# Optimization experiments

Hardware: AMD Instinct MI355X
Metric: run time of the kernel (lower is better)

Reference implementation:

```python
import jax, jax.numpy as jnp
import numpy as np

N, C, CI, H, W = 64, 512, 256, 12, 4
EPS = 1e-5


def _conv1x1(v, w, b=None):
    # v: [n, cin, h, w], w: [cout, cin]
    o = jnp.einsum('nchw,oc->nohw', v, w)
    if b is not None:
        o = o + b[None, :, None, None]
    return o


def _layernorm(v, g, b):
    # normalize over (C, H, W) per sample, affine params shaped [C, H, W]
    mu = v.mean(axis=(1, 2, 3), keepdims=True)
    var = v.var(axis=(1, 2, 3), keepdims=True)
    return (v - mu) / jnp.sqrt(var + EPS) * g[None] + b[None]


def setup_inputs() -> dict:
    key = jax.random.key(0)
    ks = jax.random.split(key, 12)
    s = 0.02
    return {
        'x': jax.random.normal(ks[0], (N, C, H, W), dtype=jnp.float32),
        'theta_w': jax.random.normal(ks[1], (CI, C), dtype=jnp.float32) * s,
        'theta_b': jnp.zeros((CI,), dtype=jnp.float32),
        'phi_w': jax.random.normal(ks[2], (CI, C), dtype=jnp.float32) * s,
        'phi_b': jnp.zeros((CI,), dtype=jnp.float32),
        'conv1_w': jax.random.normal(ks[3], (C, C), dtype=jnp.float32) * s,
        'conv2_w': jax.random.normal(ks[4], (C, C), dtype=jnp.float32) * s,
        'ln1_g': jnp.ones((C, H, W), dtype=jnp.float32),
        'ln1_b': jnp.zeros((C, H, W), dtype=jnp.float32),
        'ln2_g': jnp.ones((C, H, W), dtype=jnp.float32),
        'ln2_b': jnp.zeros((C, H, W), dtype=jnp.float32),
    }


def reference(x, theta_w, theta_b, phi_w, phi_b, conv1_w, conv2_w,
              ln1_g, ln1_b, ln2_g, ln2_b):
    n = x.shape[0]
    hw = H * W
    # 1x1 conv projections (conv is per-sample, so compute once on the N nodes
    # instead of on the N^2 gathered copies -- identical math)
    theta = _conv1x1(x, theta_w, theta_b)          # [N, CI, H, W]  (gallery proj)
    phi = _conv1x1(x, phi_w, phi_b)                # [N, CI, H, W]  (query proj)
    # MaxPool2d(2,2) on phi -> [N, CI, 6, 2] -> [N, CI, 12]
    phi_p = phi.reshape(n, CI, H // 2, 2, W // 2, 2).max(axis=(3, 5))
    phi_p = phi_p.reshape(n, CI, -1)               # [N, CI, 12]
    t = theta.reshape(n, CI, hw).transpose(0, 2, 1)  # [N, HW, CI]
    # f[i, j] = theta(x[j]) @ pooled phi(x[i]), norm='size' divides by 12
    f = jnp.einsum('jsc,icm->ijsm', t, phi_p) / phi_p.shape[-1]  # [Nq, Ng, HW, 12]
    m = f.max(axis=-1)                             # [Nq, Ng, HW]; max instead of softmax-sum
    # all-pairs layout p = i*N + j: qs[p] = i, gs[p] = j (torch.where row-major)
    gs = jnp.tile(jnp.arange(n), n)                # [N*N]
    # masked gallery image z = x[gs] * attention map, then scatter_add over gs
    z = x[gs] * m.reshape(n * n, 1, H, W)          # [N*N, C, H, W]
    x2 = jax.ops.segment_sum(z, gs, num_segments=n)
    # postprocessing (dropouts are identity at p=0)
    x = x2 + x                                     # res1
    x = _layernorm(x, ln1_g, ln1_b)
    h = _conv1x1(jax.nn.relu(_conv1x1(x, conv1_w)), conv2_w)
    x = x + h                                      # res2
    x = _layernorm(x, ln2_g, ln2_b)
    return x
```

## Files before the change

### kernel.cpp

```cpp
#include <hip/hip_runtime.h>
#include <hip/hip_bf16.h>

#define NN 64
#define CC 512
#define HW 48
#define LNSZ (CC * HW)

typedef __attribute__((ext_vector_type(8))) short bf16x8;
typedef __attribute__((ext_vector_type(4))) float floatx4;

static const size_t WB_OFF   = 0;
static const size_t BC_OFF   = 393216;
static const size_t S_OFF    = 393728;
static const size_t SMU_OFF  = 396800;
static const size_t SRS_OFF  = 396864;
static const size_t CXP_OFF  = 396928;
static const size_t CX2_OFF  = 409216;
static const size_t ST2_OFF  = 421504;
static const size_t XB_OFF   = 422016;
static const size_t TP_OFF   = 1208448;
static const size_t YB_OFF   = 1994880;
static const size_t UB_OFF   = 2781312;
static const size_t PP_OFF   = 3567744;
static const size_t YY_OFF   = 3666048;
static const size_t VV_OFF   = 5238912;

__device__ __forceinline__ void block_reduce2(float& sum, float& sq) {
  const int lane = threadIdx.x & 63, w = threadIdx.x >> 6;
#pragma unroll
  for (int off = 32; off > 0; off >>= 1) {
    sum += __shfl_down(sum, off, 64);
    sq  += __shfl_down(sq, off, 64);
  }
  __shared__ float rs[4], rq[4];
  if (lane == 0) { rs[w] = sum; rq[w] = sq; }
  __syncthreads();
  if (threadIdx.x == 0) {
    sum = rs[0] + rs[1] + rs[2] + rs[3];
    sq  = rq[0] + rq[1] + rq[2] + rq[3];
  }
}

__global__ __launch_bounds__(256) void prep_w(
    const float* __restrict__ tw, const float* __restrict__ pw,
    const float* __restrict__ c1, const float* __restrict__ c2,
    const float* __restrict__ tb, const float* __restrict__ pb,
    __hip_bfloat16* __restrict__ Wb, float* __restrict__ bcat,
    float* __restrict__ S) {
  int g = blockIdx.x * 256 + threadIdx.x;
  float v;
  if (g < 131072)      v = tw[g];
  else if (g < 262144) v = pw[g - 131072];
  else if (g < 524288) v = c1[g - 262144];
  else                 v = c2[g - 524288];
  Wb[g] = __float2bfloat16(v);
  if (g < 512) bcat[g] = g < 256 ? tb[g] : pb[g - 256];
  if (g < 3072) S[g] = 0.f;
}

__global__ __launch_bounds__(256) void trx_stats(
    const float* __restrict__ x, __hip_bfloat16* __restrict__ xb,
    float* __restrict__ cxp, float* __restrict__ cx2p) {
  const int bx = blockIdx.x;
  const int n  = blockIdx.y;
  const int t  = threadIdx.x;
  __shared__ float ts[128 * 49];
  __shared__ float ps[192], pq[192];
  const float* src = x + (size_t)n * LNSZ + (size_t)bx * 128 * HW;
#pragma unroll
  for (int k = 0; k < 6; ++k) {
    int idx = t + k * 256;
    float4 v = ((const float4*)src)[idx];
    int c = idx / 12, sq = (idx % 12) * 4;
    float* d = ts + c * 49 + sq;
    d[0] = v.x; d[1] = v.y; d[2] = v.z; d[3] = v.w;
  }
  __syncthreads();
  if (t < 192) {
    int s = t % 48, q = t / 48;
    float sum = 0.f, sq2 = 0.f;
#pragma unroll
    for (int c = q * 32; c < q * 32 + 32; ++c) {
      float v = ts[c * 49 + s];
      sum += v; sq2 += v * v;
    }
    ps[t] = sum; pq[t] = sq2;
  }
  __hip_bfloat16* dst = xb + (size_t)n * LNSZ + bx * 128;
#pragma unroll
  for (int k = 0; k < 12; ++k) {
    int idx = t + k * 256;
    int s = idx >> 6, cp = idx & 63;
    __hip_bfloat162 p;
    p.x = __float2bfloat16(ts[(cp * 2) * 49 + s]);
    p.y = __float2bfloat16(ts[(cp * 2 + 1) * 49 + s]);
    *(__hip_bfloat162*)(dst + (size_t)s * 512 + cp * 2) = p;
  }
  __syncthreads();
  if (t < 48) {
    cxp[((size_t)n * 4 + bx) * 48 + t] = ps[t] + ps[48 + t] + ps[96 + t] + ps[144 + t];
    cx2p[((size_t)n * 4 + bx) * 48 + t] = pq[t] + pq[48 + t] + pq[96 + t] + pq[144 + t];
  }
}

__global__ __launch_bounds__(256) void gemm_bf16out(
    const __hip_bfloat16* __restrict__ Wb, const __hip_bfloat16* __restrict__ inb,
    const float* __restrict__ bias, __hip_bfloat16* __restrict__ outb, int relu) {
  const int oc = blockIdx.x, n = blockIdx.y;
  const int w = threadIdx.x >> 6, lane = threadIdx.x & 63;
  const int c16 = lane & 15, quad = lane >> 4;
  const int obase = oc * 128 + w * 32;

  const __hip_bfloat16* A0 = Wb + (size_t)(obase + c16) * 512 + quad * 8;
  const __hip_bfloat16* A1 = A0 + 16 * 512;
  const __hip_bfloat16* B0 = inb + (size_t)n * LNSZ + (size_t)c16 * 512 + quad * 8;

  floatx4 zero = {0.f, 0.f, 0.f, 0.f};
  floatx4 acc[2][3];
#pragma unroll
  for (int i = 0; i < 2; ++i)
#pragma unroll
    for (int j = 0; j < 3; ++j) acc[i][j] = zero;

  bf16x8 a[2], b[3];
  a[0] = *(const bf16x8*)(A0);
  a[1] = *(const bf16x8*)(A1);
  b[0] = *(const bf16x8*)(B0);
  b[1] = *(const bf16x8*)(B0 + 16 * 512);
  b[2] = *(const bf16x8*)(B0 + 32 * 512);

  for (int k = 0; k < 480; k += 32) {
    bf16x8 an[2], bn[3];
    const int k2 = k + 32;
    an[0] = *(const bf16x8*)(A0 + k2);
    an[1] = *(const bf16x8*)(A1 + k2);
    bn[0] = *(const bf16x8*)(B0 + k2);
    bn[1] = *(const bf16x8*)(B0 + 16 * 512 + k2);
    bn[2] = *(const bf16x8*)(B0 + 32 * 512 + k2);
#pragma unroll
    for (int i = 0; i < 2; ++i)
#pragma unroll
      for (int j = 0; j < 3; ++j)
        acc[i][j] = __builtin_amdgcn_mfma_f32_16x16x32_bf16(a[i], b[j],
                                                            acc[i][j], 0, 0, 0);
    a[0] = an[0]; a[1] = an[1];
    b[0] = bn[0]; b[1] = bn[1]; b[2] = bn[2];
  }
#pragma unroll
  for (int i = 0; i < 2; ++i)
#pragma unroll
    for (int j = 0; j < 3; ++j)
      acc[i][j] = __builtin_amdgcn_mfma_f32_16x16x32_bf16(a[i], b[j],
                                                          acc[i][j], 0, 0, 0);

  __hip_bfloat16* on = outb + (size_t)n * LNSZ;
#pragma unroll
  for (int i = 0; i < 2; ++i) {
    const int o0 = obase + i * 16 + quad * 4;
    float bv[4];
#pragma unroll
    for (int r = 0; r < 4; ++r) bv[r] = bias ? bias[o0 + r] : 0.f;
#pragma unroll
    for (int j = 0; j < 3; ++j) {
      const int s = j * 16 + c16;
      union { short4 s4; __hip_bfloat16 h[4]; } u;
#pragma unroll
      for (int r = 0; r < 4; ++r) {
        float v = acc[i][j][r] + bv[r];
        if (relu) v = fmaxf(v, 0.f);
        u.h[r] = __float2bfloat16(v);
      }
      *(short4*)(on + (size_t)s * 512 + o0) = u.s4;
    }
  }
}

__global__ __launch_bounds__(256) void make_pp(
    const __hip_bfloat16* __restrict__ ThPhi, __hip_bfloat16* __restrict__ Pp) {
  int g = blockIdx.x * 256 + threadIdx.x;
  int ci = g & 255;
  int rest = g >> 8;
  int m = rest % 12, i = rest / 12;
  int sb = (m >> 1) * 8 + (m & 1) * 2;
  const __hip_bfloat16* base = ThPhi + (size_t)i * LNSZ + 256 + ci;
  float mx = __bfloat162float(base[(size_t)(sb + 0) * 512]);
  mx = fmaxf(mx, __bfloat162float(base[(size_t)(sb + 1) * 512]));
  mx = fmaxf(mx, __bfloat162float(base[(size_t)(sb + 4) * 512]));
  mx = fmaxf(mx, __bfloat162float(base[(size_t)(sb + 5) * 512]));
  Pp[g] = __float2bfloat16(mx);
}

__global__ __launch_bounds__(256) void dgemm_fused(
    const __hip_bfloat16* __restrict__ A, const __hip_bfloat16* __restrict__ B,
    float* __restrict__ S) {
  const int bn = blockIdx.x * 48;
  const int w = threadIdx.x >> 6, lane = threadIdx.x & 63;
  const int c16 = lane & 15, quad = lane >> 4;
  const int bm = blockIdx.y * 128 + w * 32;

  const __hip_bfloat16* A0 = A + (size_t)(bm + c16) * 512 + quad * 8;
  const __hip_bfloat16* A1 = A0 + 16 * 512;
  const __hip_bfloat16* Bp = B + (size_t)(bn + c16) * 256 + quad * 8;

  floatx4 zero = {0.f, 0.f, 0.f, 0.f};
  floatx4 acc[2][3];
#pragma unroll
  for (int i = 0; i < 2; ++i)
#pragma unroll
    for (int j = 0; j < 3; ++j) acc[i][j] = zero;

#pragma unroll 2
  for (int k = 0; k < 256; k += 32) {
    bf16x8 a0 = *(const bf16x8*)(A0 + k);
    bf16x8 a1 = *(const bf16x8*)(A1 + k);
    bf16x8 b0 = *(const bf16x8*)(Bp + k);
    bf16x8 b1 = *(const bf16x8*)(Bp + 16 * 256 + k);
    bf16x8 b2 = *(const bf16x8*)(Bp + 32 * 256 + k);
    acc[0][0] = __builtin_amdgcn_mfma_f32_16x16x32_bf16(a0, b0, acc[0][0], 0, 0, 0);
    acc[0][1] = __builtin_amdgcn_mfma_f32_16x16x32_bf16(a0, b1, acc[0][1], 0, 0, 0);
    acc[0][2] = __builtin_amdgcn_mfma_f32_16x16x32_bf16(a0, b2, acc[0][2], 0, 0, 0);
    acc[1][0] = __builtin_amdgcn_mfma_f32_16x16x32_bf16(a1, b0, acc[1][0], 0, 0, 0);
    acc[1][1] = __builtin_amdgcn_mfma_f32_16x16x32_bf16(a1, b1, acc[1][1], 0, 0, 0);
    acc[1][2] = __builtin_amdgcn_mfma_f32_16x16x32_bf16(a1, b2, acc[1][2], 0, 0, 0);
  }

  __shared__ float red[4 * 48 * 33];
  float* rw = red + w * (48 * 33);
#pragma unroll
  for (int i = 0; i < 2; ++i)
#pragma unroll
    for (int j = 0; j < 3; ++j)
#pragma unroll
      for (int r = 0; r < 4; ++r)
        rw[(j * 16 + c16) * 33 + (i * 16 + quad * 4 + r)] = acc[i][j][r];
  __syncthreads();
  if (lane < 32) {
    float sum = 0.f;
#pragma unroll
    for (int grp = 0; grp < 4; ++grp) {
      float mx = rw[(grp * 12) * 33 + lane];
#pragma unroll
      for (int m = 1; m < 12; ++m)
        mx = fmaxf(mx, rw[(grp * 12 + m) * 33 + lane]);
      sum += mx;
    }
    atomicAdd(&S[bm + lane], sum * (1.0f / 12.0f));
  }
}

__global__ __launch_bounds__(64) void ln1_finish(
    const float* __restrict__ S, const float* __restrict__ cxp,
    const float* __restrict__ cx2p, float* __restrict__ smu,
    float* __restrict__ srstd) {
  const int n = blockIdx.x, lane = threadIdx.x;
  float sum = 0.f, sq = 0.f;
  if (lane < 48) {
    float a = 1.0f + S[n * 48 + lane];
    float c1 = 0.f, c2 = 0.f;
#pragma unroll
    for (int ch = 0; ch < 4; ++ch) {
      c1 += cxp[((size_t)n * 4 + ch) * 48 + lane];
      c2 += cx2p[((size_t)n * 4 + ch) * 48 + lane];
    }
    sum = a * c1;
    sq = a * a * c2;
  }
#pragma unroll
  for (int off = 32; off > 0; off >>= 1) {
    sum += __shfl_down(sum, off, 64);
    sq  += __shfl_down(sq, off, 64);
  }
  if (lane == 0) {
    float mu = sum * (1.0f / LNSZ);
    float var = sq * (1.0f / LNSZ) - mu * mu;
    smu[n] = mu;
    srstd[n] = 1.0f / sqrtf(var + 1e-5f);
  }
}

__global__ __launch_bounds__(256) void ln1_norm_tr(
    const float* __restrict__ x, const float* __restrict__ S,
    const float* __restrict__ smu, const float* __restrict__ srstd,
    const float* __restrict__ g, const float* __restrict__ b,
    float* __restrict__ y, __hip_bfloat16* __restrict__ yb) {
  const int bx = blockIdx.x, n = blockIdx.y, t = threadIdx.x;
  __shared__ float ts[128 * 49];
  __shared__ float sS[HW];
  if (t < HW) sS[t] = 1.0f + S[n * HW + t];
  __syncthreads();
  const float mu = smu[n], rstd = srstd[n];
  const size_t chunk = (size_t)bx * 6144;
  const float* xn = x + (size_t)n * LNSZ + chunk;
  float* yn = y + (size_t)n * LNSZ + chunk;
  const float* gp = g + chunk;
  const float* bp = b + chunk;
#pragma unroll
  for (int k = 0; k < 6; ++k) {
    int idx = t + k * 256;
    int c = idx / 12, sq0 = (idx % 12) * 4;
    float4 xv = ((const float4*)xn)[idx];
    float4 gv = ((const float4*)gp)[idx];
    float4 bv = ((const float4*)bp)[idx];
    float4 o;
    o.x = (xv.x * sS[sq0]     - mu) * rstd * gv.x + bv.x;
    o.y = (xv.y * sS[sq0 + 1] - mu) * rstd * gv.y + bv.y;
    o.z = (xv.z * sS[sq0 + 2] - mu) * rstd * gv.z + bv.z;
    o.w = (xv.w * sS[sq0 + 3] - mu) * rstd * gv.w + bv.w;
    ((float4*)yn)[idx] = o;
    float* d = ts + c * 49 + sq0;
    d[0] = o.x; d[1] = o.y; d[2] = o.z; d[3] = o.w;
  }
  __syncthreads();
  __hip_bfloat16* dst = yb + (size_t)n * LNSZ + bx * 128;
#pragma unroll
  for (int k = 0; k < 12; ++k) {
    int idx = t + k * 256;
    int s = idx >> 6, cp = idx & 63;
    __hip_bfloat162 p;
    p.x = __float2bfloat16(ts[(cp * 2) * 49 + s]);
    p.y = __float2bfloat16(ts[(cp * 2 + 1) * 49 + s]);
    *(__hip_bfloat162*)(dst + (size_t)s * 512 + cp * 2) = p;
  }
}

__global__ __launch_bounds__(256) void conv2_fused(
    const __hip_bfloat16* __restrict__ Wb, const __hip_bfloat16* __restrict__ inb,
    const float* __restrict__ y, float* __restrict__ v,
    float2* __restrict__ stats2) {
  const int oc = blockIdx.x, n = blockIdx.y;
  const int w = threadIdx.x >> 6, lane = threadIdx.x & 63;
  const int c16 = lane & 15, quad = lane >> 4;
  const int obase = oc * 128 + w * 32;

  const __hip_bfloat16* A0 = Wb + (size_t)(obase + c16) * 512 + quad * 8;
  const __hip_bfloat16* A1 = A0 + 16 * 512;
  const __hip_bfloat16* B0 = inb + (size_t)n * LNSZ + (size_t)c16 * 512 + quad * 8;

  floatx4 zero = {0.f, 0.f, 0.f, 0.f};
  floatx4 acc[2][3];
#pragma unroll
  for (int i = 0; i < 2; ++i)
#pragma unroll
    for (int j = 0; j < 3; ++j) acc[i][j] = zero;

  bf16x8 a[2], b[3];
  a[0] = *(const bf16x8*)(A0);
  a[1] = *(const bf16x8*)(A1);
  b[0] = *(const bf16x8*)(B0);
  b[1] = *(const bf16x8*)(B0 + 16 * 512);
  b[2] = *(const bf16x8*)(B0 + 32 * 512);

  for (int k = 0; k < 480; k += 32) {
    bf16x8 an[2], bn[3];
    const int k2 = k + 32;
    an[0] = *(const bf16x8*)(A0 + k2);
    an[1] = *(const bf16x8*)(A1 + k2);
    bn[0] = *(const bf16x8*)(B0 + k2);
    bn[1] = *(const bf16x8*)(B0 + 16 * 512 + k2);
    bn[2] = *(const bf16x8*)(B0 + 32 * 512 + k2);
#pragma unroll
    for (int i = 0; i < 2; ++i)
#pragma unroll
      for (int j = 0; j < 3; ++j)
        acc[i][j] = __builtin_amdgcn_mfma_f32_16x16x32_bf16(a[i], b[j],
                                                            acc[i][j], 0, 0, 0);
    a[0] = an[0]; a[1] = an[1];
    b[0] = bn[0]; b[1] = bn[1]; b[2] = bn[2];
  }
#pragma unroll
  for (int i = 0; i < 2; ++i)
#pragma unroll
    for (int j = 0; j < 3; ++j)
      acc[i][j] = __builtin_amdgcn_mfma_f32_16x16x32_bf16(a[i], b[j],
                                                          acc[i][j], 0, 0, 0);

  const float* yn = y + (size_t)n * LNSZ;
  float* vn = v + (size_t)n * LNSZ;
  float sum = 0.f, sq = 0.f;
#pragma unroll
  for (int i = 0; i < 2; ++i)
#pragma unroll
    for (int r = 0; r < 4; ++r) {
      const int o = obase + i * 16 + quad * 4 + r;
#pragma unroll
      for (int j = 0; j < 3; ++j) {
        const int s = j * 16 + c16;
        float val = acc[i][j][r] + yn[(size_t)o * HW + s];
        vn[(size_t)o * HW + s] = val;
        sum += val;
        sq += val * val;
      }
    }
  block_reduce2(sum, sq);
  if (threadIdx.x == 0) stats2[n * 4 + oc] = make_float2(sum, sq);
}

__global__ __launch_bounds__(256) void ln2_norm(
    const float* __restrict__ v, const float2* __restrict__ stats2,
    const float* __restrict__ g2, const float* __restrict__ b2,
    float* __restrict__ out) {
  const int bx = blockIdx.x, n = blockIdx.y, t = threadIdx.x;
  __shared__ float smu, srstd;
  if (t == 0) {
    float s1 = 0.f, s2 = 0.f;
#pragma unroll
    for (int k = 0; k < 4; ++k) {
      float2 p = stats2[n * 4 + k];
      s1 += p.x; s2 += p.y;
    }
    float mu = s1 * (1.0f / LNSZ);
    float var = s2 * (1.0f / LNSZ) - mu * mu;
    smu = mu;
    srstd = 1.0f / sqrtf(var + 1e-5f);
  }
  __syncthreads();
  const float mu = smu, rstd = srstd;
  const size_t chunk = (size_t)bx * 6144;
  const float* vn = v + (size_t)n * LNSZ + chunk;
  float* on = out + (size_t)n * LNSZ + chunk;
  const float* gp = g2 + chunk;
  const float* bp = b2 + chunk;
#pragma unroll
  for (int k = 0; k < 6; ++k) {
    int idx = t + k * 256;
    float4 vv = ((const float4*)vn)[idx];
    float4 gv = ((const float4*)gp)[idx];
    float4 bv = ((const float4*)bp)[idx];
    float4 o;
    o.x = (vv.x - mu) * rstd * gv.x + bv.x;
    o.y = (vv.y - mu) * rstd * gv.y + bv.y;
    o.z = (vv.z - mu) * rstd * gv.z + bv.z;
    o.w = (vv.w - mu) * rstd * gv.w + bv.w;
    ((float4*)on)[idx] = o;
  }
}

extern "C" void kernel_launch(void* const* d_in, const int* in_sizes, int n_in,
                              void* d_out, int out_size, void* d_ws, size_t ws_size,
                              hipStream_t stream) {
  const float* x   = (const float*)d_in[0];
  const float* tw  = (const float*)d_in[1];
  const float* tb  = (const float*)d_in[2];
  const float* pw  = (const float*)d_in[3];
  const float* pb  = (const float*)d_in[4];
  const float* c1w = (const float*)d_in[5];
  const float* c2w = (const float*)d_in[6];
  const float* g1  = (const float*)d_in[7];
  const float* b1  = (const float*)d_in[8];
  const float* g2  = (const float*)d_in[9];
  const float* b2  = (const float*)d_in[10];

  float* ws = (float*)d_ws;
  __hip_bfloat16* Wb = (__hip_bfloat16*)(ws + WB_OFF);
  float* bcat        = ws + BC_OFF;
  float* S           = ws + S_OFF;
  float* smu         = ws + SMU_OFF;
  float* srstd       = ws + SRS_OFF;
  float* cxp         = ws + CXP_OFF;
  float* cx2p        = ws + CX2_OFF;
  float2* st2        = (float2*)(ws + ST2_OFF);
  __hip_bfloat16* xb = (__hip_bfloat16*)(ws + XB_OFF);
  __hip_bfloat16* tp = (__hip_bfloat16*)(ws + TP_OFF);
  __hip_bfloat16* yb = (__hip_bfloat16*)(ws + YB_OFF);
  __hip_bfloat16* ub = (__hip_bfloat16*)(ws + UB_OFF);
  __hip_bfloat16* Pp = (__hip_bfloat16*)(ws + PP_OFF);
  float* y           = ws + YY_OFF;
  float* v           = ws + VV_OFF;
  float* out         = (float*)d_out;

  prep_w<<<3072, 256, 0, stream>>>(tw, pw, c1w, c2w, tb, pb, Wb, bcat, S);
  trx_stats<<<dim3(4, NN), 256, 0, stream>>>(x, xb, cxp, cx2p);
  gemm_bf16out<<<dim3(4, NN), 256, 0, stream>>>(Wb, xb, bcat, tp, 0);
  make_pp<<<768, 256, 0, stream>>>(tp, Pp);
  dgemm_fused<<<dim3(16, 24), 256, 0, stream>>>(tp, Pp, S);
  ln1_finish<<<NN, 64, 0, stream>>>(S, cxp, cx2p, smu, srstd);
  ln1_norm_tr<<<dim3(4, NN), 256, 0, stream>>>(x, S, smu, srstd, g1, b1, y, yb);
  gemm_bf16out<<<dim3(4, NN), 256, 0, stream>>>(Wb + 512 * 512, yb, nullptr, ub, 1);
  conv2_fused<<<dim3(4, NN), 256, 0, stream>>>(Wb + 1024 * 512, ub, y, v, st2);
  ln2_norm<<<dim3(4, NN), 256, 0, stream>>>(v, st2, g2, b2, out);
}
```

Measured before the change: 141.1 us.

## Fuse weight prep, pooling, and LN1 finish into neighboring kernels

New measurement: 135.9 us, median of 2. -3.7%, faster.

```diff
diff --git a/kernel.cpp b/kernel.cpp
--- a/kernel.cpp
+++ b/kernel.cpp
@@ -12,8 +12,6 @@
 static const size_t WB_OFF   = 0;
 static const size_t BC_OFF   = 393216;
 static const size_t S_OFF    = 393728;
-static const size_t SMU_OFF  = 396800;
-static const size_t SRS_OFF  = 396864;
 static const size_t CXP_OFF  = 396928;
 static const size_t CX2_OFF  = 409216;
 static const size_t ST2_OFF  = 421504;
@@ -41,31 +39,38 @@
   }
 }
 
-__global__ __launch_bounds__(256) void prep_w(
+__global__ __launch_bounds__(256) void prep_all(
     const float* __restrict__ tw, const float* __restrict__ pw,
     const float* __restrict__ c1, const float* __restrict__ c2,
     const float* __restrict__ tb, const float* __restrict__ pb,
+    const float* __restrict__ x,
     __hip_bfloat16* __restrict__ Wb, float* __restrict__ bcat,
-    float* __restrict__ S) {
-  int g = blockIdx.x * 256 + threadIdx.x;
-  float v;
-  if (g < 131072)      v = tw[g];
-  else if (g < 262144) v = pw[g - 131072];
-  else if (g < 524288) v = c1[g - 262144];
-  else                 v = c2[g - 524288];
-  Wb[g] = __float2bfloat16(v);
-  if (g < 512) bcat[g] = g < 256 ? tb[g] : pb[g - 256];
-  if (g < 3072) S[g] = 0.f;
-}
-
-__global__ __launch_bounds__(256) void trx_stats(
-    const float* __restrict__ x, __hip_bfloat16* __restrict__ xb,
+    float* __restrict__ S, __hip_bfloat16* __restrict__ xb,
     float* __restrict__ cxp, float* __restrict__ cx2p) {
-  const int bx = blockIdx.x;
-  const int n  = blockIdx.y;
-  const int t  = threadIdx.x;
   __shared__ float ts[128 * 49];
   __shared__ float ps[192], pq[192];
+  if (blockIdx.x < 768) {
+    int g = blockIdx.x * 256 + threadIdx.x;
+    float4 v;
+    if (g < 32768)       v = ((const float4*)tw)[g];
+    else if (g < 65536)  v = ((const float4*)pw)[g - 32768];
+    else if (g < 131072) v = ((const float4*)c1)[g - 65536];
+    else                 v = ((const float4*)c2)[g - 131072];
+    union { short4 s4; __hip_bfloat16 h[4]; } u;
+    u.h[0] = __float2bfloat16(v.x);
+    u.h[1] = __float2bfloat16(v.y);
+    u.h[2] = __float2bfloat16(v.z);
+    u.h[3] = __float2bfloat16(v.w);
+    ((short4*)Wb)[g] = u.s4;
+    if (g < 64)       ((float4*)bcat)[g] = ((const float4*)tb)[g];
+    else if (g < 128) ((float4*)bcat)[g] = ((const float4*)pb)[g - 64];
+    if (g < 768) ((float4*)S)[g] = make_float4(0.f, 0.f, 0.f, 0.f);
+    return;
+  }
+  const int bb = blockIdx.x - 768;
+  const int bx = bb & 3;
+  const int n  = bb >> 2;
+  const int t  = threadIdx.x;
   const float* src = x + (size_t)n * LNSZ + (size_t)bx * 128 * HW;
 #pragma unroll
   for (int k = 0; k < 6; ++k) {
@@ -105,7 +110,8 @@
 
 __global__ __launch_bounds__(256) void gemm_bf16out(
     const __hip_bfloat16* __restrict__ Wb, const __hip_bfloat16* __restrict__ inb,
-    const float* __restrict__ bias, __hip_bfloat16* __restrict__ outb, int relu) {
+    const float* __restrict__ bias, __hip_bfloat16* __restrict__ outb, int relu,
+    __hip_bfloat16* __restrict__ Pp) {
   const int oc = blockIdx.x, n = blockIdx.y;
   const int w = threadIdx.x >> 6, lane = threadIdx.x & 63;
   const int c16 = lane & 15, quad = lane >> 4;
@@ -153,6 +159,9 @@
       acc[i][j] = __builtin_amdgcn_mfma_f32_16x16x32_bf16(a[i], b[j],
                                                           acc[i][j], 0, 0, 0);
 
+  __shared__ float pt[128 * 49];
+  const int do_pp = (Pp != nullptr) && (oc >= 2);
+
   __hip_bfloat16* on = outb + (size_t)n * LNSZ;
 #pragma unroll
   for (int i = 0; i < 2; ++i) {
@@ -169,25 +178,23 @@
         float v = acc[i][j][r] + bv[r];
         if (relu) v = fmaxf(v, 0.f);
         u.h[r] = __float2bfloat16(v);
+        if (do_pp) pt[(w * 32 + i * 16 + quad * 4 + r) * 49 + s] = v;
       }
       *(short4*)(on + (size_t)s * 512 + o0) = u.s4;
     }
   }
-}
-
-__global__ __launch_bounds__(256) void make_pp(
-    const __hip_bfloat16* __restrict__ ThPhi, __hip_bfloat16* __restrict__ Pp) {
-  int g = blockIdx.x * 256 + threadIdx.x;
-  int ci = g & 255;
-  int rest = g >> 8;
-  int m = rest % 12, i = rest / 12;
-  int sb = (m >> 1) * 8 + (m & 1) * 2;
-  const __hip_bfloat16* base = ThPhi + (size_t)i * LNSZ + 256 + ci;
-  float mx = __bfloat162float(base[(size_t)(sb + 0) * 512]);
-  mx = fmaxf(mx, __bfloat162float(base[(size_t)(sb + 1) * 512]));
-  mx = fmaxf(mx, __bfloat162float(base[(size_t)(sb + 4) * 512]));
-  mx = fmaxf(mx, __bfloat162float(base[(size_t)(sb + 5) * 512]));
-  Pp[g] = __float2bfloat16(mx);
+  if (do_pp) {
+    __syncthreads();
+#pragma unroll
+    for (int rep = 0; rep < 6; ++rep) {
+      int idx = threadIdx.x + rep * 256;
+      int m = idx >> 7, cil = idx & 127;
+      int sb = (m >> 1) * 8 + (m & 1) * 2;
+      const float* pr = pt + cil * 49;
+      float mx = fmaxf(fmaxf(pr[sb], pr[sb + 1]), fmaxf(pr[sb + 4], pr[sb + 5]));
+      Pp[((size_t)(n * 12 + m) << 8) + (oc - 2) * 128 + cil] = __float2bfloat16(mx);
+    }
+  }
 }
 
 __global__ __launch_bounds__(256) void dgemm_fused(
@@ -248,47 +255,43 @@
   }
 }
 
-__global__ __launch_bounds__(64) void ln1_finish(
-    const float* __restrict__ S, const float* __restrict__ cxp,
-    const float* __restrict__ cx2p, float* __restrict__ smu,
-    float* __restrict__ srstd) {
-  const int n = blockIdx.x, lane = threadIdx.x;
-  float sum = 0.f, sq = 0.f;
-  if (lane < 48) {
-    float a = 1.0f + S[n * 48 + lane];
-    float c1 = 0.f, c2 = 0.f;
-#pragma unroll
-    for (int ch = 0; ch < 4; ++ch) {
-      c1 += cxp[((size_t)n * 4 + ch) * 48 + lane];
-      c2 += cx2p[((size_t)n * 4 + ch) * 48 + lane];
-    }
-    sum = a * c1;
-    sq = a * a * c2;
-  }
-#pragma unroll
-  for (int off = 32; off > 0; off >>= 1) {
-    sum += __shfl_down(sum, off, 64);
-    sq  += __shfl_down(sq, off, 64);
-  }
-  if (lane == 0) {
-    float mu = sum * (1.0f / LNSZ);
-    float var = sq * (1.0f / LNSZ) - mu * mu;
-    smu[n] = mu;
-    srstd[n] = 1.0f / sqrtf(var + 1e-5f);
-  }
-}
-
 __global__ __launch_bounds__(256) void ln1_norm_tr(
     const float* __restrict__ x, const float* __restrict__ S,
-    const float* __restrict__ smu, const float* __restrict__ srstd,
+    const float* __restrict__ cxp, const float* __restrict__ cx2p,
     const float* __restrict__ g, const float* __restrict__ b,
     float* __restrict__ y, __hip_bfloat16* __restrict__ yb) {
   const int bx = blockIdx.x, n = blockIdx.y, t = threadIdx.x;
   __shared__ float ts[128 * 49];
   __shared__ float sS[HW];
+  __shared__ float sstat[2];
   if (t < HW) sS[t] = 1.0f + S[n * HW + t];
-  __syncthreads();
-  const float mu = smu[n], rstd = srstd[n];
+  if (t < 64) {
+    float sum = 0.f, sq = 0.f;
+    if (t < 48) {
+      float a = 1.0f + S[n * HW + t];
+      float c1 = 0.f, c2 = 0.f;
+#pragma unroll
+      for (int ch = 0; ch < 4; ++ch) {
+        c1 += cxp[((size_t)n * 4 + ch) * 48 + t];
+        c2 += cx2p[((size_t)n * 4 + ch) * 48 + t];
+      }
+      sum = a * c1;
+      sq = a * a * c2;
+    }
+#pragma unroll
+    for (int off = 32; off > 0; off >>= 1) {
+      sum += __shfl_down(sum, off, 64);
+      sq  += __shfl_down(sq, off, 64);
+    }
+    if (t == 0) {
+      float mu = sum * (1.0f / LNSZ);
+      float var = sq * (1.0f / LNSZ) - mu * mu;
+      sstat[0] = mu;
+      sstat[1] = 1.0f / sqrtf(var + 1e-5f);
+    }
+  }
+  __syncthreads();
+  const float mu = sstat[0], rstd = sstat[1];
   const size_t chunk = (size_t)bx * 6144;
   const float* xn = x + (size_t)n * LNSZ + chunk;
   float* yn = y + (size_t)n * LNSZ + chunk;
@@ -454,8 +457,6 @@
   __hip_bfloat16* Wb = (__hip_bfloat16*)(ws + WB_OFF);
   float* bcat        = ws + BC_OFF;
   float* S           = ws + S_OFF;
-  float* smu         = ws + SMU_OFF;
-  float* srstd       = ws + SRS_OFF;
   float* cxp         = ws + CXP_OFF;
   float* cx2p        = ws + CX2_OFF;
   float2* st2        = (float2*)(ws + ST2_OFF);
@@ -468,14 +469,13 @@
   float* v           = ws + VV_OFF;
   float* out         = (float*)d_out;
 
-  prep_w<<<3072, 256, 0, stream>>>(tw, pw, c1w, c2w, tb, pb, Wb, bcat, S);
-  trx_stats<<<dim3(4, NN), 256, 0, stream>>>(x, xb, cxp, cx2p);
-  gemm_bf16out<<<dim3(4, NN), 256, 0, stream>>>(Wb, xb, bcat, tp, 0);
-  make_pp<<<768, 256, 0, stream>>>(tp, Pp);
+  prep_all<<<1024, 256, 0, stream>>>(tw, pw, c1w, c2w, tb, pb, x,
+                                     Wb, bcat, S, xb, cxp, cx2p);
+  gemm_bf16out<<<dim3(4, NN), 256, 0, stream>>>(Wb, xb, bcat, tp, 0, Pp);
   dgemm_fused<<<dim3(16, 24), 256, 0, stream>>>(tp, Pp, S);
-  ln1_finish<<<NN, 64, 0, stream>>>(S, cxp, cx2p, smu, srstd);
-  ln1_norm_tr<<<dim3(4, NN), 256, 0, stream>>>(x, S, smu, srstd, g1, b1, y, yb);
-  gemm_bf16out<<<dim3(4, NN), 256, 0, stream>>>(Wb + 512 * 512, yb, nullptr, ub, 1);
+  ln1_norm_tr<<<dim3(4, NN), 256, 0, stream>>>(x, S, cxp, cx2p, g1, b1, y, yb);
+  gemm_bf16out<<<dim3(4, NN), 256, 0, stream>>>(Wb + 512 * 512, yb, nullptr, ub, 1,
+                                                nullptr);
   conv2_fused<<<dim3(4, NN), 256, 0, stream>>>(Wb + 1024 * 512, ub, y, v, st2);
   ln2_norm<<<dim3(4, NN), 256, 0, stream>>>(v, st2, g2, b2, out);
 }
```
